# Performance work log

Measured on AMD Instinct MI355X. Metric: run time of the kernel, lower is better.

Reference implementation:

```python
import jax, jax.numpy as jnp
import numpy as np
from jax import lax

IN_CH = 512
OUT_CH = 512
KERNEL = 3
STYLE_DIM = 512
BATCH = 8
HW = 64
EPS = 1e-08
LR_MUL = 1.0


def setup_inputs() -> dict:
    key = jax.random.key(0)
    k1, k2, k3, k4 = jax.random.split(key, 4)
    x = jax.random.normal(k1, (BATCH, IN_CH, HW, HW), dtype=jnp.float32)
    style = jax.random.normal(k2, (BATCH, STYLE_DIM), dtype=jnp.float32)
    weight = jax.random.normal(k3, (1, OUT_CH, IN_CH, KERNEL, KERNEL), dtype=jnp.float32)
    mod_weight = jax.random.normal(k4, (IN_CH, STYLE_DIM), dtype=jnp.float32)
    mod_bias = jnp.ones((IN_CH,), dtype=jnp.float32)  # bias_init=1
    return {"x": x, "style": style, "weight": weight,
            "mod_weight": mod_weight, "mod_bias": mod_bias}


def reference(x, style, weight, mod_weight, mod_bias):
    batch, in_ch, h, w_dim = x.shape
    conv_scale = 1.0 / np.sqrt(in_ch * KERNEL * KERNEL)
    lin_scale = 1.0 / np.sqrt(STYLE_DIM) * LR_MUL

    # EqualizedLinear modulation: style -> per-channel scale, shape (B, in_ch)
    s = style @ (mod_weight * lin_scale).T + mod_bias * LR_MUL

    # Modulate: (B, out, in, k, k)
    w = conv_scale * weight * s[:, None, :, None, None]
    # Demodulate
    demod = lax.rsqrt(jnp.sum(w * w, axis=(2, 3, 4)) + EPS)  # (B, out)
    w = w * demod[:, :, None, None, None]

    pad = KERNEL // 2

    def conv_one(xi, wi):
        # xi: (in, H, W), wi: (out, in, k, k)
        return lax.conv_general_dilated(
            xi[None], wi, window_strides=(1, 1),
            padding=[(pad, pad), (pad, pad)],
            dimension_numbers=("NCHW", "OIHW", "NCHW"))[0]

    out = jax.vmap(conv_one)(x, w)  # (B, out, H, W)
    return out
```

## Files before the change

kernel.cpp:

```cpp
#include <hip/hip_runtime.h>
#include <hip/hip_bf16.h>
#include <cstdint>

#define IN_CH 512
#define OUT_CH 512
#define STYLE_DIM 512
#define BATCH 8
#define HW 64

typedef __bf16 bf16x8 __attribute__((ext_vector_type(8)));
typedef float f32x16 __attribute__((ext_vector_type(16)));

__device__ __forceinline__ void gload_lds16(const void* g, void* l) {
  __builtin_amdgcn_global_load_lds(
      (const __attribute__((address_space(1))) unsigned int*)g,
      (__attribute__((address_space(3))) unsigned int*)l,
      16, 0, 0);
}

#define WAITV(N) asm volatile("s_waitcnt vmcnt(" #N ")" ::: "memory")
#define BARRIER() do { asm volatile("" ::: "memory"); __builtin_amdgcn_s_barrier(); \
                       asm volatile("" ::: "memory"); } while (0)

__global__ void k_style(const float* __restrict__ style, const float* __restrict__ modw,
                        const float* __restrict__ modb, float* __restrict__ s_out) {
  __shared__ float st[BATCH * STYLE_DIM];
  const int tid = threadIdx.x;
  for (int i = tid; i < BATCH * STYLE_DIM; i += 256) st[i] = style[i];
  __syncthreads();
  const int ic = blockIdx.x * 4 + (tid >> 6);
  const int l = tid & 63;
  const float* mr = modw + (size_t)ic * STYLE_DIM + l * 8;
  float m[8];
  #pragma unroll
  for (int j = 0; j < 8; ++j) m[j] = mr[j];
  float accs[8];
  #pragma unroll
  for (int b = 0; b < 8; ++b) {
    const float* sb = st + b * STYLE_DIM + l * 8;
    float a = 0.f;
    #pragma unroll
    for (int j = 0; j < 8; ++j) a += m[j] * sb[j];
    accs[b] = a;
  }
  #pragma unroll
  for (int off = 32; off; off >>= 1) {
    #pragma unroll
    for (int b = 0; b < 8; ++b) accs[b] += __shfl_down(accs[b], off, 64);
  }
  if (l == 0) {
    #pragma unroll
    for (int b = 0; b < 8; ++b)
      s_out[b * IN_CH + ic] = accs[b] * 0.04419417382415922f + modb[ic];
  }
}

__global__ void k_wprep(const float* __restrict__ w, float* __restrict__ wsq,
                        __bf16* __restrict__ wb) {
  const int idx = blockIdx.x * 256 + threadIdx.x;
  const int oc = idx >> 9, ic = idx & 511;
  const float* p = w + ((size_t)oc * IN_CH + ic) * 9;
  const int icw = ic ^ ((oc & 7) << 3);
  float sum = 0.f;
  #pragma unroll
  for (int t = 0; t < 9; ++t) {
    float v = p[t];
    sum += v * v;
    wb[((size_t)(t * OUT_CH) + oc) * IN_CH + icw] = (__bf16)v;
  }
  wsq[oc * IN_CH + ic] = sum;
}

__global__ void k_demod(const float* __restrict__ s, const float* __restrict__ wsq,
                        float* __restrict__ scale) {
  const int oc = blockIdx.x;
  const int l = threadIdx.x;
  const float* wr = wsq + (size_t)oc * IN_CH + l * 8;
  float w8[8];
  #pragma unroll
  for (int j = 0; j < 8; ++j) w8[j] = wr[j];
  #pragma unroll
  for (int b = 0; b < 8; ++b) {
    const float* sb = s + b * IN_CH + l * 8;
    float acc = 0.f;
    #pragma unroll
    for (int j = 0; j < 8; ++j) { float sv = sb[j]; acc += sv * sv * w8[j]; }
    #pragma unroll
    for (int off = 32; off; off >>= 1) acc += __shfl_down(acc, off, 64);
    if (l == 0)
      scale[b * OUT_CH + oc] =
          rsqrtf(acc * (1.0f / 4608.0f) + 1e-8f) * 0.014731391274719732f;
  }
}

__global__ void k_xprep(const float* __restrict__ x, const float* __restrict__ s,
                        __bf16* __restrict__ xg) {
  const int b = blockIdx.x >> 6, y = blockIdx.x & 63;
  const int w = threadIdx.x >> 6, lane = threadIdx.x & 63;
  const float* sr = s + b * IN_CH;
  #pragma unroll
  for (int it = 0; it < 8; ++it) {
    const int ug = it * 8 + w;
    bf16x8 pk;
    #pragma unroll
    for (int j = 0; j < 8; ++j) {
      const int ic = ug * 8 + j;
      pk[j] = (__bf16)(x[(((size_t)(b * IN_CH) + ic) * HW + y) * HW + lane] * sr[ic]);
    }
    *(bf16x8*)(xg + ((((size_t)(b * 64 + ug) * HW + y) * HW + lane) * 8)) = pk;
  }
}

__global__ __launch_bounds__(512, 2) void k_conv(
    const __bf16* __restrict__ Wg,
    const __bf16* __restrict__ Xg,
    const float* __restrict__ scale,
    float* __restrict__ out)
{
  __shared__ __attribute__((aligned(16))) __bf16 Xs[6 * 66 * 64];
  __shared__ __attribute__((aligned(16))) __bf16 Wl[3][256 * 64];
  __shared__ __attribute__((aligned(16))) __bf16 Dump[1024];

  const int tid = threadIdx.x;
  const int lane = tid & 63;
  const int wid = tid >> 6;
  const int wm = wid >> 2;
  const int wn = wid & 3;
  const int ln31 = lane & 31;
  const int laneK = lane >> 5;

  const int bid0 = blockIdx.x;
  const int bid = (bid0 & 7) * 32 + (bid0 >> 3);
  const int octile = bid & 1;
  const int ptile = (bid >> 1) & 15;
  const int b = bid >> 5;
  const int oc0 = octile * 256;
  const int r0 = ptile * 4;

  auto stage_w = [&](int chunkv, int tapv, int bsel) {
    const int ic0 = chunkv * 64;
    #pragma unroll
    for (int i = 0; i < 4; ++i) {
      const int sidx = tid + 512 * i;
      const int oc = sidx >> 3, u = sidx & 7;
      gload_lds16(Wg + (((size_t)(tapv * OUT_CH) + oc0 + oc) * IN_CH + ic0 + u * 8),
                  &Wl[bsel][oc * 64 + u * 8]);
    }
  };
  auto stage_x = [&](int chunkv) {
    const int col = tid >> 3;
    const int u = tid & 7;
    const int ug = chunkv * 8 + (u ^ ((col + 1) & 7));
    #pragma unroll
    for (int j = 0; j < 6; ++j) {
      const int y = r0 - 1 + j;
      const bool ok = (y >= 0 && y < HW);
      const int yc = ok ? y : 0;
      void* dst = ok ? (void*)&Xs[(j * 66 + col + 1) * 64 + u * 8]
                     : (void*)&Dump[(tid & 127) * 8];
      gload_lds16(Xg + ((((size_t)(b * 64 + ug) * HW + yc) * HW + col) * 8), dst);
    }
  };

  {
    float4 z = {0.f, 0.f, 0.f, 0.f};
    float4* p = (float4*)Xs;
    for (int i = tid; i < 6 * 66 * 64 / 8; i += 512) p[i] = z;
  }
  __syncthreads();
  stage_x(0);
  stage_w(0, 0, 0);
  stage_w(0, 1, 1);

  const int kb = laneK * 8;
  const int akey8 = (ln31 & 7) << 3;
  int aoffe[4];
  #pragma unroll
  for (int ks = 0; ks < 4; ++ks) aoffe[ks] = (ks * 16 + kb) ^ akey8;
  int bele[3][4];
  #pragma unroll
  for (int dxi = 0; dxi < 3; ++dxi) {
    const int bkey8 = ((ln31 + dxi) & 7) << 3;
    #pragma unroll
    for (int ks = 0; ks < 4; ++ks) bele[dxi][ks] = (ks * 16 + kb) ^ bkey8;
  }
  const __bf16* __restrict__ wbp0 = &Wl[0][(128 * wm + ln31) * 64];
  const __bf16* __restrict__ wbp1 = wbp0 + 256 * 64;
  const __bf16* __restrict__ wbp2 = wbp1 + 256 * 64;
  const __bf16* __restrict__ xwb = &Xs[((wn + 1) * 66 + (ln31 + 1)) * 64];

  f32x16 acc[4][2] = {};

#define TAPBODY(T) { \
    if ((T) == 8 && c == 7) { WAITV(0); } else { WAITV(4); } \
    BARRIER(); \
    const __bf16* __restrict__ wbase = ((T) % 3 == 0) ? wbp0 : ((T) % 3 == 1) ? wbp1 : wbp2; \
    const __bf16* __restrict__ xb0 = xwb + (((T) / 3 - 1) * 66 + ((T) % 3 - 1)) * 64; \
    _Pragma("unroll") \
    for (int ks = 0; ks < 4; ++ks) { \
      const int ael = aoffe[ks]; \
      const int bel = bele[(T) % 3][ks]; \
      bf16x8 av[4], bv[2]; \
      _Pragma("unroll") \
      for (int mf = 0; mf < 4; ++mf) av[mf] = *(const bf16x8*)(wbase + mf * 2048 + ael); \
      bv[0] = *(const bf16x8*)(xb0 + bel); \
      bv[1] = *(const bf16x8*)(xb0 + 32 * 64 + bel); \
      __builtin_amdgcn_s_setprio(1); \
      _Pragma("unroll") \
      for (int mf = 0; mf < 4; ++mf) { \
        acc[mf][0] = __builtin_amdgcn_mfma_f32_32x32x16_bf16(av[mf], bv[0], acc[mf][0], 0, 0, 0); \
        acc[mf][1] = __builtin_amdgcn_mfma_f32_32x32x16_bf16(av[mf], bv[1], acc[mf][1], 0, 0, 0); \
      } \
      __builtin_amdgcn_s_setprio(0); \
    } \
    if ((T) == 8) { \
      if (c < 7) { BARRIER(); stage_x(c + 1); stage_w(c + 1, 1, 1); } \
    } else if ((T) <= 6) { \
      stage_w(c, (T) + 2, ((T) + 2) % 3); \
    } else {  \
      if (c < 7) stage_w(c + 1, 0, 0); \
    } \
  }

  #pragma unroll 1
  for (int c = 0; c < 8; ++c) {
    TAPBODY(0) TAPBODY(1) TAPBODY(2)
    TAPBODY(3) TAPBODY(4) TAPBODY(5)
    TAPBODY(6) TAPBODY(7) TAPBODY(8)
  }

  const int y = r0 + wn;
  #pragma unroll
  for (int mf = 0; mf < 4; ++mf) {
    #pragma unroll
    for (int reg = 0; reg < 16; ++reg) {
      const int rowid = (reg & 3) + 8 * (reg >> 2) + 4 * laneK;
      const int oc = oc0 + 128 * wm + 32 * mf + rowid;
      const float sc = scale[b * OUT_CH + oc];
      float* op = out + (((size_t)(b * OUT_CH + oc) * HW + y) * HW) + ln31;
      op[0] = acc[mf][0][reg] * sc;
      op[32] = acc[mf][1][reg] * sc;
    }
  }
}

extern "C" void kernel_launch(void* const* d_in, const int* in_sizes, int n_in,
                              void* d_out, int out_size, void* d_ws, size_t ws_size,
                              hipStream_t stream) {
  const float* x      = (const float*)d_in[0];
  const float* style  = (const float*)d_in[1];
  const float* weight = (const float*)d_in[2];
  const float* modw   = (const float*)d_in[3];
  const float* modb   = (const float*)d_in[4];
  float* out = (float*)d_out;

  char* ws = (char*)d_ws;
  float*  s_buf = (float*)(ws + 0);
  float*  scale = (float*)(ws + 16384);
  float*  wsq   = (float*)(ws + 32768);
  __bf16* wb    = (__bf16*)(ws + 32768 + 1048576);
  __bf16* xg    = (__bf16*)(ws + 32768 + 1048576 + 9 * OUT_CH * IN_CH * 2);

  k_style<<<128, 256, 0, stream>>>(style, modw, modb, s_buf);
  k_wprep<<<1024, 256, 0, stream>>>(weight, wsq, wb);
  k_demod<<<512, 64, 0, stream>>>(s_buf, wsq, scale);
  k_xprep<<<BATCH * HW, 512, 0, stream>>>(x, s_buf, xg);
  k_conv<<<256, 512, 0, stream>>>(wb, xg, scale, out);
}
```

Measured before the change: 170.8 us.

## Re-swizzle LDS layout for weights and input tile, load padding zeros from global

Replaces the XOR swizzle applied in the weight prep kernel and the LDS addressing with a new pairwise-row, rotated-slot layout for both the weight and input tiles in shared memory, computed during staging rather than pre-baked in global memory. Halo and out-of-range input rows are now fetched from a small zeroed global buffer instead of zero-filling LDS up front and dumping invalid loads, which removes the initial LDS clear and its barrier. The aim is fewer LDS bank conflicts on the MFMA operand reads and a shorter prologue. It adds a memset and per-load index arithmetic including a division by 66.

```diff
diff --git a/kernel.cpp b/kernel.cpp
--- a/kernel.cpp
+++ b/kernel.cpp
@@ -60,13 +60,12 @@
   const int idx = blockIdx.x * 256 + threadIdx.x;
   const int oc = idx >> 9, ic = idx & 511;
   const float* p = w + ((size_t)oc * IN_CH + ic) * 9;
-  const int icw = ic ^ ((oc & 7) << 3);
   float sum = 0.f;
   #pragma unroll
   for (int t = 0; t < 9; ++t) {
     float v = p[t];
     sum += v * v;
-    wb[((size_t)(t * OUT_CH) + oc) * IN_CH + icw] = (__bf16)v;
+    wb[((size_t)(t * OUT_CH) + oc) * IN_CH + ic] = (__bf16)v;
   }
   wsq[oc * IN_CH + ic] = sum;
 }
@@ -115,11 +114,11 @@
     const __bf16* __restrict__ Wg,
     const __bf16* __restrict__ Xg,
     const float* __restrict__ scale,
+    const __bf16* __restrict__ zpg,
     float* __restrict__ out)
 {
-  __shared__ __attribute__((aligned(16))) __bf16 Xs[6 * 66 * 64];
-  __shared__ __attribute__((aligned(16))) __bf16 Wl[3][256 * 64];
-  __shared__ __attribute__((aligned(16))) __bf16 Dump[1024];
+  __shared__ __attribute__((aligned(16))) __bf16 Xs[3584 * 8];
+  __shared__ __attribute__((aligned(16))) __bf16 Wl[3][2048 * 8];
 
   const int tid = threadIdx.x;
   const int lane = tid & 63;
@@ -128,6 +127,7 @@
   const int wn = wid & 3;
   const int ln31 = lane & 31;
   const int laneK = lane >> 5;
+  const int kord = wid & 3;
 
   const int bid0 = blockIdx.x;
   const int bid = (bid0 & 7) * 32 + (bid0 >> 3);
@@ -138,73 +138,65 @@
   const int r0 = ptile * 4;
 
   auto stage_w = [&](int chunkv, int tapv, int bsel) {
-    const int ic0 = chunkv * 64;
     #pragma unroll
     for (int i = 0; i < 4; ++i) {
-      const int sidx = tid + 512 * i;
-      const int oc = sidx >> 3, u = sidx & 7;
-      gload_lds16(Wg + (((size_t)(tapv * OUT_CH) + oc0 + oc) * IN_CH + ic0 + u * 8),
-                  &Wl[bsel][oc * 64 + u * 8]);
+      const int u = i * 512 + tid;
+      const int j = u >> 4, p = u & 15;
+      const int row = 2 * j + (p & 1);
+      const int s = ((p >> 1) - j) & 7;
+      gload_lds16(Wg + (((size_t)(tapv * OUT_CH) + oc0 + row) * IN_CH + chunkv * 64 + s * 8),
+                  (void*)((char*)Wl[bsel] + u * 16));
     }
   };
   auto stage_x = [&](int chunkv) {
-    const int col = tid >> 3;
-    const int u = tid & 7;
-    const int ug = chunkv * 8 + (u ^ ((col + 1) & 7));
-    #pragma unroll
-    for (int j = 0; j < 6; ++j) {
-      const int y = r0 - 1 + j;
-      const bool ok = (y >= 0 && y < HW);
-      const int yc = ok ? y : 0;
-      void* dst = ok ? (void*)&Xs[(j * 66 + col + 1) * 64 + u * 8]
-                     : (void*)&Dump[(tid & 127) * 8];
-      gload_lds16(Xg + ((((size_t)(b * 64 + ug) * HW + yc) * HW + col) * 8), dst);
+    #pragma unroll
+    for (int i = 0; i < 7; ++i) {
+      const int u = i * 512 + tid;
+      const int j = u >> 4, p = u & 15;
+      const int R = 2 * j + (p & 1);
+      const int s = ((p >> 1) - j) & 7;
+      const int xrow = (int)((unsigned)R / 66u);
+      const int col = R - 66 * xrow;
+      const int y = r0 - 1 + xrow;
+      const bool ok = (col >= 1) & (col <= 64) & (y >= 0) & (y < HW);
+      const __bf16* src = ok
+          ? Xg + ((((size_t)(b * 64 + chunkv * 8 + s) * HW + y) * HW + (col - 1)) * 8)
+          : zpg;
+      gload_lds16(src, (void*)((char*)Xs + u * 16));
     }
   };
 
-  {
-    float4 z = {0.f, 0.f, 0.f, 0.f};
-    float4* p = (float4*)Xs;
-    for (int i = tid; i < 6 * 66 * 64 / 8; i += 512) p[i] = z;
-  }
-  __syncthreads();
   stage_x(0);
   stage_w(0, 0, 0);
   stage_w(0, 1, 1);
 
-  const int kb = laneK * 8;
-  const int akey8 = (ln31 & 7) << 3;
-  int aoffe[4];
-  #pragma unroll
-  for (int ks = 0; ks < 4; ++ks) aoffe[ks] = (ks * 16 + kb) ^ akey8;
-  int bele[3][4];
-  #pragma unroll
-  for (int dxi = 0; dxi < 3; ++dxi) {
-    const int bkey8 = ((ln31 + dxi) & 7) << 3;
-    #pragma unroll
-    for (int ks = 0; ks < 4; ++ks) bele[dxi][ks] = (ks * 16 + kb) ^ bkey8;
-  }
-  const __bf16* __restrict__ wbp0 = &Wl[0][(128 * wm + ln31) * 64];
-  const __bf16* __restrict__ wbp1 = wbp0 + 256 * 64;
-  const __bf16* __restrict__ wbp2 = wbp1 + 256 * 64;
-  const __bf16* __restrict__ xwb = &Xs[((wn + 1) * 66 + (ln31 + 1)) * 64];
+  const int keyA = ln31 + 2 * laneK + 4 * kord;
+  int aoff8[4];
+  #pragma unroll
+  for (int ks = 0; ks < 4; ++ks) aoff8[ks] = ((keyA + 4 * ks) & 15) * 8;
+  const __bf16* __restrict__ ab0 = Wl[0] + (64 * wm + (ln31 >> 1)) * 128;
+  const __bf16* __restrict__ ab1 = Wl[1] + (64 * wm + (ln31 >> 1)) * 128;
+  const __bf16* __restrict__ ab2 = Wl[2] + (64 * wm + (ln31 >> 1)) * 128;
+  const int RB = wn * 66 + ln31;
+  const int kB0 = RB + 2 * laneK + 4 * kord;
 
   f32x16 acc[4][2] = {};
 
 #define TAPBODY(T) { \
     if ((T) == 8 && c == 7) { WAITV(0); } else { WAITV(4); } \
     BARRIER(); \
-    const __bf16* __restrict__ wbase = ((T) % 3 == 0) ? wbp0 : ((T) % 3 == 1) ? wbp1 : wbp2; \
-    const __bf16* __restrict__ xb0 = xwb + (((T) / 3 - 1) * 66 + ((T) % 3 - 1)) * 64; \
+    const __bf16* __restrict__ abase = ((T) % 3 == 0) ? ab0 : ((T) % 3 == 1) ? ab1 : ab2; \
+    const int Rt = RB + ((T) / 3) * 66 + ((T) % 3); \
+    const int kBt = kB0 + ((T) / 3) * 66 + ((T) % 3); \
+    const __bf16* __restrict__ xbase = Xs + (Rt >> 1) * 128; \
     _Pragma("unroll") \
     for (int ks = 0; ks < 4; ++ks) { \
-      const int ael = aoffe[ks]; \
-      const int bel = bele[(T) % 3][ks]; \
+      const int bp = ((kBt + 4 * ks) & 15) * 8; \
       bf16x8 av[4], bv[2]; \
       _Pragma("unroll") \
-      for (int mf = 0; mf < 4; ++mf) av[mf] = *(const bf16x8*)(wbase + mf * 2048 + ael); \
-      bv[0] = *(const bf16x8*)(xb0 + bel); \
-      bv[1] = *(const bf16x8*)(xb0 + 32 * 64 + bel); \
+      for (int mf = 0; mf < 4; ++mf) av[mf] = *(const bf16x8*)(abase + mf * 2048 + aoff8[ks]); \
+      bv[0] = *(const bf16x8*)(xbase + bp); \
+      bv[1] = *(const bf16x8*)(xbase + 2048 + bp); \
       __builtin_amdgcn_s_setprio(1); \
       _Pragma("unroll") \
       for (int mf = 0; mf < 4; ++mf) { \
@@ -257,13 +249,15 @@
   char* ws = (char*)d_ws;
   float*  s_buf = (float*)(ws + 0);
   float*  scale = (float*)(ws + 16384);
-  float*  wsq   = (float*)(ws + 32768);
-  __bf16* wb    = (__bf16*)(ws + 32768 + 1048576);
-  __bf16* xg    = (__bf16*)(ws + 32768 + 1048576 + 9 * OUT_CH * IN_CH * 2);
-
+  __bf16* zpg   = (__bf16*)(ws + 32768);
+  float*  wsq   = (float*)(ws + 36864);
+  __bf16* wb    = (__bf16*)(ws + 36864 + 1048576);
+  __bf16* xg    = (__bf16*)(ws + 36864 + 1048576 + 9 * OUT_CH * IN_CH * 2);
+
+  hipMemsetAsync(zpg, 0, 4096, stream);
   k_style<<<128, 256, 0, stream>>>(style, modw, modb, s_buf);
   k_wprep<<<1024, 256, 0, stream>>>(weight, wsq, wb);
   k_demod<<<512, 64, 0, stream>>>(s_buf, wsq, scale);
   k_xprep<<<BATCH * HW, 512, 0, stream>>>(x, s_buf, xg);
-  k_conv<<<256, 512, 0, stream>>>(wb, xg, scale, out);
-}
+  k_conv<<<256, 512, 0, stream>>>(wb, xg, scale, zpg, out);
+}
```

Result: slower. 200.1 us (+17.2%).
